# Performance work log

Hardware: AMD Instinct MI355X
Metric: run time of the kernel (lower is better)

Reference implementation:

```python
import jax, jax.numpy as jnp
import numpy as np

B, S, D, F, TOPK = 8, 2048, 1024, 64, 8


def setup_inputs() -> dict:
    key = jax.random.key(0)
    ks = jax.random.split(key, 4)
    scale = 1.0 / np.sqrt(D)
    return {
        "x": jax.random.normal(ks[0], (B, S, D), dtype=jnp.float32),
        "W_top": jax.random.normal(ks[1], (D, F), dtype=jnp.float32) * scale,
        "b_top": jnp.zeros((F,), dtype=jnp.float32),
        "W_feat": jax.random.normal(ks[2], (D, F), dtype=jnp.float32) * scale,
        "b_feat": jnp.zeros((F,), dtype=jnp.float32),
        "W_gates": jax.random.normal(ks[3], (F, D), dtype=jnp.float32) * scale,
        "b_gates": jnp.zeros((F,), dtype=jnp.float32),
        "alpha": jnp.ones((1,), dtype=jnp.float32),
        "num": TOPK,
    }


def reference(x, W_top, b_top, W_feat, b_feat, W_gates, b_gates, alpha, num):
    # Router logits and top-k selection: [B,S,F] -> vals/idx [B,S,num]
    top_logits = jnp.einsum("bsd,df->bsf", x, W_top) + b_top
    vals, idx = jax.lax.top_k(top_logits, num)
    sm = jax.nn.softmax(vals, axis=-1)                     # softmax over selected experts
    # Scatter softmax'd top-k weights into dense [B,S,F] (zeros elsewhere)
    onehot = jax.nn.one_hot(idx, F, dtype=sm.dtype)        # [B,S,num,F]
    type_dense = jnp.einsum("bsk,bskf->bsf", sm, onehot)
    # Dense softmax routing branch
    feat_soft = jax.nn.softmax(jnp.einsum("bsd,df->bsf", x, W_feat) + b_feat, axis=-1)
    a = jax.nn.sigmoid(alpha)                              # [1], broadcasts
    features = a * type_dense + (1.0 - a) * feat_soft      # [B,S,F]
    # num_feature small Linear(dims,1)+Sigmoid gates fused into one GEMM
    gates = jax.nn.sigmoid(jnp.einsum("bsd,fd->bsf", x, W_gates) + b_gates)  # [B,S,F]
    # Weighted sum over feature axis; original returns shape [B,S,1]
    return jnp.sum(gates * features, axis=-1, keepdims=True)
```

## Files before the change

### kernel.cpp

```cpp
#include <hip/hip_runtime.h>
#include <math.h>

#define D_DIM 1024
#define TOKB  32
#define KCH   16

typedef short  bf16x8 __attribute__((ext_vector_type(8)));
typedef float  f32x4  __attribute__((ext_vector_type(4)));

__device__ __forceinline__ ushort f2bf(float f) {
  uint u = __float_as_uint(f);
  return (ushort)((u + 0x7fffu + ((u >> 16) & 1u)) >> 16);
}
__device__ __forceinline__ float bf2f(ushort h) {
  return __uint_as_float(((uint)h) << 16);
}
__device__ __forceinline__ float sigm(float v) {
  return 1.f / (1.f + expf(-v));
}
__device__ __forceinline__ void conv8(const f32x4 va, const f32x4 vb,
                                      bf16x8& ah, bf16x8& al) {
#pragma unroll
  for (int i = 0; i < 8; ++i) {
    float v = (i < 4) ? va[i] : vb[i - 4];
    ushort h = f2bf(v);
    ah[i] = (short)h;
    al[i] = (short)f2bf(v - bf2f(h));
  }
}

__global__ __launch_bounds__(256) void pack_w_kernel(
    const float* __restrict__ Wt, const float* __restrict__ Wf,
    const float* __restrict__ Wg, ushort* __restrict__ Wp) {
  int gid = blockIdx.x * 256 + threadIdx.x;
  if (gid >= 32 * 12 * 64 * 4) return;
  int jp   = gid & 3;
  int t    = gid >> 2;
  int lane = t & 63;
  int t2   = t >> 6;
  int fb   = t2 % 12;
  int ks   = t2 / 12;
  int k0   = ks * 32 + ((lane >> 4) << 3) + jp * 2;
  int f    = fb * 16 + (lane & 15);
  float v0, v1;
  if (f < 64)       { v0 = Wt[k0 * 64 + f];            v1 = Wt[(k0 + 1) * 64 + f]; }
  else if (f < 128) { v0 = Wf[k0 * 64 + f - 64];       v1 = Wf[(k0 + 1) * 64 + f - 64]; }
  else              { v0 = Wg[(f - 128) * D_DIM + k0]; v1 = Wg[(f - 128) * D_DIM + k0 + 1]; }
  ushort h0 = f2bf(v0), h1 = f2bf(v1);
  ushort l0 = f2bf(v0 - bf2f(h0)), l1 = f2bf(v1 - bf2f(h1));
  size_t base = ((size_t)(ks * 12 + fb) * 2) * 512 + lane * 8 + jp * 2;
  *(uint*)(Wp + base)       = (uint)h0 | ((uint)h1 << 16);
  *(uint*)(Wp + base + 512) = (uint)l0 | ((uint)l1 << 16);
}

__global__ __launch_bounds__(256, 2) void moe_gate_kernel(
    const float* __restrict__ x, const ushort* __restrict__ Wp,
    const float* __restrict__ b_top, const float* __restrict__ b_feat,
    const float* __restrict__ b_gates, const float* __restrict__ alpha,
    const int* __restrict__ nump, float* __restrict__ out) {
  __shared__ float L[32 * 196 + 192];
  float* bsm = L + 32 * 196;
  const int tid  = threadIdx.x;
  const int lane = tid & 63;
  const int wid  = tid >> 6;
  const int kh   = wid >> 1;
  const int wc   = wid & 1;
  const int tok0 = blockIdx.x * TOKB;

  if (tid < 192)
    bsm[tid] = (tid < 64) ? b_top[tid]
             : (tid < 128) ? b_feat[tid - 64] : b_gates[tid - 128];

  const float* xp0 = x + (size_t)(tok0 + (lane & 15)) * D_DIM + kh * 512 + ((lane >> 4) << 3);
  const float* xp1 = xp0 + (size_t)16 * D_DIM;
  const ushort* wbase = Wp + (size_t)(kh * KCH) * 12288 + (size_t)(wc * 6) * 1024 + lane * 8;

  f32x4 acc[2][6] = {};
  bf16x8 bAh[6], bAl[6], bBh[6], bBl[6];
  f32x4 xA[4], xB[4];

#define LOADB(BH, BL, c) do {                                        \
    const ushort* wp_ = wbase + (size_t)(c) * 12288;                 \
    _Pragma("unroll")                                                \
    for (int q = 0; q < 6; ++q) {                                    \
      BH[q] = *(const bf16x8*)(wp_ + q * 1024);                      \
      BL[q] = *(const bf16x8*)(wp_ + q * 1024 + 512);                \
    } } while (0)
#define LOADX(XR, c) do {                                            \
    XR[0] = *(const f32x4*)(xp0 + (c) * 32);                         \
    XR[1] = *(const f32x4*)(xp0 + (c) * 32 + 4);                     \
    XR[2] = *(const f32x4*)(xp1 + (c) * 32);                         \
    XR[3] = *(const f32x4*)(xp1 + (c) * 32 + 4); } while (0)
#define COMPUTE(XR, BH, BL) do {                                     \
    bf16x8 ah0, al0, ah1, al1;                                       \
    conv8(XR[0], XR[1], ah0, al0);                                   \
    conv8(XR[2], XR[3], ah1, al1);                                   \
    _Pragma("unroll")                                                \
    for (int q = 0; q < 6; ++q) {                                    \
      acc[0][q] = __builtin_amdgcn_mfma_f32_16x16x32_bf16(ah0, BH[q], acc[0][q], 0, 0, 0); \
      acc[0][q] = __builtin_amdgcn_mfma_f32_16x16x32_bf16(al0, BH[q], acc[0][q], 0, 0, 0); \
      acc[0][q] = __builtin_amdgcn_mfma_f32_16x16x32_bf16(ah0, BL[q], acc[0][q], 0, 0, 0); \
      acc[1][q] = __builtin_amdgcn_mfma_f32_16x16x32_bf16(ah1, BH[q], acc[1][q], 0, 0, 0); \
      acc[1][q] = __builtin_amdgcn_mfma_f32_16x16x32_bf16(al1, BH[q], acc[1][q], 0, 0, 0); \
      acc[1][q] = __builtin_amdgcn_mfma_f32_16x16x32_bf16(ah1, BL[q], acc[1][q], 0, 0, 0); \
    } } while (0)

  LOADB(bAh, bAl, 0);
  LOADX(xA, 0);
  for (int c = 0; c < KCH; c += 2) {
    LOADB(bBh, bBl, c + 1);
    LOADX(xB, c + 1);
    COMPUTE(xA, bAh, bAl);
    if (c + 2 < KCH) {
      LOADB(bAh, bAl, c + 2);
      LOADX(xA, c + 2);
    }
    COMPUTE(xB, bBh, bBl);
  }
#undef LOADB
#undef LOADX
#undef COMPUTE

  __syncthreads();
  if (kh == 0) {
#pragma unroll
    for (int tf = 0; tf < 2; ++tf)
#pragma unroll
      for (int q = 0; q < 6; ++q) {
        int f = wc * 96 + q * 16 + (lane & 15);
        int t = tf * 16 + ((lane >> 4) << 2);
        float bv = bsm[f];
#pragma unroll
        for (int r = 0; r < 4; ++r)
          L[(t + r) * 196 + f] = acc[tf][q][r] + bv;
      }
  }
  __syncthreads();
  if (kh == 1) {
#pragma unroll
    for (int tf = 0; tf < 2; ++tf)
#pragma unroll
      for (int q = 0; q < 6; ++q) {
        int f = wc * 96 + q * 16 + (lane & 15);
        int t = tf * 16 + ((lane >> 4) << 2);
#pragma unroll
        for (int r = 0; r < 4; ++r)
          L[(t + r) * 196 + f] += acc[tf][q][r];
      }
  }
  __syncthreads();

  {
    const int t   = tid >> 3;
    const int sub = tid & 7;
    const float* Lr = L + t * 196;
    float tp[8], ftv[8], gtv[8];
#pragma unroll
    for (int j = 0; j < 8; ++j) {
      int f = sub + 8 * j;
      tp[j]  = Lr[f];
      ftv[j] = Lr[64 + f];
      gtv[j] = sigm(Lr[128 + f]);
    }
    float mf = ftv[0];
#pragma unroll
    for (int j = 1; j < 8; ++j) mf = fmaxf(mf, ftv[j]);
#pragma unroll
    for (int m = 1; m < 8; m <<= 1) mf = fmaxf(mf, __shfl_xor(mf, m, 8));
    float Zf = 0.f, Sf = 0.f;
#pragma unroll
    for (int j = 0; j < 8; ++j) {
      float e = expf(ftv[j] - mf);
      Zf += e;
      Sf = fmaf(gtv[j], e, Sf);
    }
#pragma unroll
    for (int m = 1; m < 8; m <<= 1) {
      Zf += __shfl_xor(Zf, m, 8);
      Sf += __shfl_xor(Sf, m, 8);
    }
    int num = *nump;
    num = num < 1 ? 1 : (num > 64 ? 64 : num);
    uint sel8 = 0;
    float m0 = 0.f, Zt = 0.f, St = 0.f;
    for (int k = 0; k < num; ++k) {
      float bv = -3.4e38f; int bj = -1;
#pragma unroll
      for (int j = 0; j < 8; ++j)
        if (!((sel8 >> j) & 1u) && tp[j] > bv) { bv = tp[j]; bj = j; }
      int bf = (bj >= 0) ? (sub + 8 * bj) : (1 << 30);
#pragma unroll
      for (int m = 1; m < 8; m <<= 1) {
        float ov = __shfl_xor(bv, m, 8);
        int   of = __shfl_xor(bf, m, 8);
        if (ov > bv || (ov == bv && of < bf)) { bv = ov; bf = of; }
      }
      if (k == 0) m0 = bv;
      float e = expf(bv - m0);
      Zt += e;
      St = fmaf(sigm(Lr[128 + bf]), e, St);
      if ((bf & 7) == sub) sel8 |= 1u << (bf >> 3);
    }
    if (sub == 0) {
      float a = sigm(alpha[0]);
      out[tok0 + t] = a * (St / Zt) + (1.f - a) * (Sf / Zf);
    }
  }
}

extern "C" void kernel_launch(void* const* d_in, const int* in_sizes, int n_in,
                              void* d_out, int out_size, void* d_ws, size_t ws_size,
                              hipStream_t stream) {
  const float* x       = (const float*)d_in[0];
  const float* W_top   = (const float*)d_in[1];
  const float* b_top   = (const float*)d_in[2];
  const float* W_feat  = (const float*)d_in[3];
  const float* b_feat  = (const float*)d_in[4];
  const float* W_gates = (const float*)d_in[5];
  const float* b_gates = (const float*)d_in[6];
  const float* alpha   = (const float*)d_in[7];
  const int*   nump    = (const int*)d_in[8];
  float*       out     = (float*)d_out;
  ushort*      Wp      = (ushort*)d_ws;

  int n_tok = in_sizes[0] / D_DIM;
  hipLaunchKernelGGL(pack_w_kernel, dim3(384), dim3(256), 0, stream,
                     W_top, W_feat, W_gates, Wp);
  hipLaunchKernelGGL(moe_gate_kernel, dim3(n_tok / TOKB), dim3(256), 0, stream,
                     x, Wp, b_top, b_feat, b_gates, alpha, nump, out);
}
```

Before: 141.0 us.

## Split K across four waves per column pair and use packed bf16 conversion

Doubles the block to 512 threads so four K-slices of 256 are processed by separate wave pairs, each running half as many chunks, with the partial sums reduced through shared memory in three serialized phases. This is meant to raise memory-level parallelism and shorten each wave's serial MFMA chain. The fp32-to-bf16 hi/lo split now uses the packed __float22bfloat162_rn intrinsic in place of manual rounding, to cut conversion ALU work. The costs are extra reduction passes with barriers, and launch bounds of 4 blocks of 512 threads, which caps registers per thread and may cause spills.

```diff
diff --git a/kernel.cpp b/kernel.cpp
--- a/kernel.cpp
+++ b/kernel.cpp
@@ -1,9 +1,10 @@
 #include <hip/hip_runtime.h>
+#include <hip/hip_bf16.h>
 #include <math.h>
 
 #define D_DIM 1024
 #define TOKB  32
-#define KCH   16
+#define NCHW  8
 
 typedef short  bf16x8 __attribute__((ext_vector_type(8)));
 typedef float  f32x4  __attribute__((ext_vector_type(4)));
@@ -20,12 +21,22 @@
 }
 __device__ __forceinline__ void conv8(const f32x4 va, const f32x4 vb,
                                       bf16x8& ah, bf16x8& al) {
-#pragma unroll
-  for (int i = 0; i < 8; ++i) {
-    float v = (i < 4) ? va[i] : vb[i - 4];
-    ushort h = f2bf(v);
-    ah[i] = (short)h;
-    al[i] = (short)f2bf(v - bf2f(h));
+  uint* AH = reinterpret_cast<uint*>(&ah);
+  uint* AL = reinterpret_cast<uint*>(&al);
+#pragma unroll
+  for (int p = 0; p < 4; ++p) {
+    float a = (p < 2) ? va[2 * p]     : vb[2 * (p - 2)];
+    float b = (p < 2) ? va[2 * p + 1] : vb[2 * (p - 2) + 1];
+    __hip_bfloat162 h2 = __float22bfloat162_rn(float2{a, b});
+    uint hu;
+    __builtin_memcpy(&hu, &h2, 4);
+    AH[p] = hu;
+    float ra = a - __uint_as_float(hu << 16);
+    float rb = b - __uint_as_float(hu & 0xffff0000u);
+    __hip_bfloat162 l2 = __float22bfloat162_rn(float2{ra, rb});
+    uint lu;
+    __builtin_memcpy(&lu, &l2, 4);
+    AL[p] = lu;
   }
 }
 
@@ -53,7 +64,7 @@
   *(uint*)(Wp + base + 512) = (uint)l0 | ((uint)l1 << 16);
 }
 
-__global__ __launch_bounds__(256, 2) void moe_gate_kernel(
+__global__ __launch_bounds__(512, 4) void moe_gate_kernel(
     const float* __restrict__ x, const ushort* __restrict__ Wp,
     const float* __restrict__ b_top, const float* __restrict__ b_feat,
     const float* __restrict__ b_gates, const float* __restrict__ alpha,
@@ -71,9 +82,9 @@
     bsm[tid] = (tid < 64) ? b_top[tid]
              : (tid < 128) ? b_feat[tid - 64] : b_gates[tid - 128];
 
-  const float* xp0 = x + (size_t)(tok0 + (lane & 15)) * D_DIM + kh * 512 + ((lane >> 4) << 3);
+  const float* xp0 = x + (size_t)(tok0 + (lane & 15)) * D_DIM + kh * 256 + ((lane >> 4) << 3);
   const float* xp1 = xp0 + (size_t)16 * D_DIM;
-  const ushort* wbase = Wp + (size_t)(kh * KCH) * 12288 + (size_t)(wc * 6) * 1024 + lane * 8;
+  const ushort* wbase = Wp + (size_t)(kh * NCHW) * 12288 + (size_t)(wc * 6) * 1024 + lane * 8;
 
   f32x4 acc[2][6] = {};
   bf16x8 bAh[6], bAl[6], bBh[6], bBl[6];
@@ -107,11 +118,11 @@
 
   LOADB(bAh, bAl, 0);
   LOADX(xA, 0);
-  for (int c = 0; c < KCH; c += 2) {
+  for (int c = 0; c < NCHW; c += 2) {
     LOADB(bBh, bBl, c + 1);
     LOADX(xB, c + 1);
     COMPUTE(xA, bAh, bAl);
-    if (c + 2 < KCH) {
+    if (c + 2 < NCHW) {
       LOADB(bAh, bAl, c + 2);
       LOADX(xA, c + 2);
     }
@@ -136,21 +147,24 @@
       }
   }
   __syncthreads();
-  if (kh == 1) {
-#pragma unroll
-    for (int tf = 0; tf < 2; ++tf)
-#pragma unroll
-      for (int q = 0; q < 6; ++q) {
-        int f = wc * 96 + q * 16 + (lane & 15);
-        int t = tf * 16 + ((lane >> 4) << 2);
-#pragma unroll
-        for (int r = 0; r < 4; ++r)
-          L[(t + r) * 196 + f] += acc[tf][q][r];
-      }
-  }
-  __syncthreads();
-
-  {
+#pragma unroll 1
+  for (int ph = 1; ph < 4; ++ph) {
+    if (kh == ph) {
+#pragma unroll
+      for (int tf = 0; tf < 2; ++tf)
+#pragma unroll
+        for (int q = 0; q < 6; ++q) {
+          int f = wc * 96 + q * 16 + (lane & 15);
+          int t = tf * 16 + ((lane >> 4) << 2);
+#pragma unroll
+          for (int r = 0; r < 4; ++r)
+            L[(t + r) * 196 + f] += acc[tf][q][r];
+        }
+    }
+    __syncthreads();
+  }
+
+  if (tid < 256) {
     const int t   = tid >> 3;
     const int sub = tid & 7;
     const float* Lr = L + t * 196;
@@ -226,6 +240,6 @@
   int n_tok = in_sizes[0] / D_DIM;
   hipLaunchKernelGGL(pack_w_kernel, dim3(384), dim3(256), 0, stream,
                      W_top, W_feat, W_gates, Wp);
-  hipLaunchKernelGGL(moe_gate_kernel, dim3(n_tok / TOKB), dim3(256), 0, stream,
+  hipLaunchKernelGGL(moe_gate_kernel, dim3(n_tok / TOKB), dim3(512), 0, stream,
                      x, Wp, b_top, b_feat, b_gates, alpha, nump, out);
 }
```

After: 242.8 us. +72.1%, slower.
